# Optimization experiments

Hardware: AMD Instinct MI355X
Metric: run time of the kernel (lower is better)

## Reference

```python
import jax, jax.numpy as jnp
import numpy as np

B, SP, SS = 8, 512, 64          # batch, prefix seq len, suffix seq len
HP, HS = 2048, 1024             # prefix / suffix hidden sizes
NH, NKV, HD = 8, 1, 256         # heads, kv heads, head dim (GQA groups = 8)
IP, IS = 16384, 4096            # MLP intermediate sizes
COND = 1024                     # adaRMSNorm conditioning dim
T = SP + SS
EPS = 1e-6
SCALE = HD ** -0.5
ROPE_BASE = 10000.0


def _rms(x):
    var = jnp.mean(jnp.square(x), axis=-1, keepdims=True)
    return x * jax.lax.rsqrt(var + EPS)


def _rot_half(x):
    x1, x2 = jnp.split(x, 2, axis=-1)
    return jnp.concatenate([-x2, x1], axis=-1)


def setup_inputs() -> dict:
    key = jax.random.key(0)
    ks = iter(jax.random.split(key, 40))
    rn = lambda shape, s=0.02: jax.random.normal(next(ks), shape, dtype=jnp.float32) * s
    return dict(
        x_prefix=rn((B, SP, HP), 1.0),
        x_suffix=rn((B, SS, HS), 1.0),
        cond=rn((B, COND), 1.0),
        attention_mask=jnp.zeros((B, 1, T, T), jnp.float32),
        p_ln1_w=rn((HP,)),
        p_q=rn((NH * HD, HP)), p_k=rn((NKV * HD, HP)), p_v=rn((NKV * HD, HP)), p_o=rn((HP, NH * HD)),
        p_ln2_w=rn((HP,)),
        p_gate=rn((IP, HP)), p_up=rn((IP, HP)), p_down=rn((HP, IP)),
        s_ada1_w=rn((3 * HS, COND)), s_ada1_b=rn((3 * HS,)),
        s_q=rn((NH * HD, HS)), s_k=rn((NKV * HD, HS)), s_v=rn((NKV * HD, HS)), s_o=rn((HS, NH * HD)),
        s_ada2_w=rn((3 * HS, COND)), s_ada2_b=rn((3 * HS,)),
        s_gate=rn((IS, HS)), s_up=rn((IS, HS)), s_down=rn((HS, IS)),
        position_ids=jnp.broadcast_to(jnp.arange(T, dtype=jnp.int32), (B, T)),
    )


def _ada_norm(x, cond, w, b):
    # AdaRMSNormV2: rms(x)*(1+scale)+shift; gate returned separately
    mod = cond @ w.T + b                      # [B, 3*HS]
    scale, shift, gate = jnp.split(mod, 3, axis=-1)
    normed = _rms(x) * (1.0 + scale[:, None, :]) + shift[:, None, :]
    return normed, gate[:, None, :]


def _qkv(h, wq, wk, wv):
    b, t, _ = h.shape
    q = (h @ wq.T).reshape(b, t, NH, HD).transpose(0, 2, 1, 3)   # [B,NH,t,HD]
    k = (h @ wk.T).reshape(b, t, NKV, HD).transpose(0, 2, 1, 3)  # [B,1,t,HD]
    v = (h @ wv.T).reshape(b, t, NKV, HD).transpose(0, 2, 1, 3)
    return q, k, v


def reference(x_prefix, x_suffix, cond, attention_mask,
              p_ln1_w, p_q, p_k, p_v, p_o, p_ln2_w, p_gate, p_up, p_down,
              s_ada1_w, s_ada1_b, s_q, s_k, s_v, s_o, s_ada2_w, s_ada2_b,
              s_gate, s_up, s_down, position_ids):
    # --- pre-attention norms ---
    hp = _rms(x_prefix) * (1.0 + p_ln1_w)                  # plain RMSNorm, gate=None
    hs, gate1 = _ada_norm(x_suffix, cond, s_ada1_w, s_ada1_b)

    qp, kp, vp = _qkv(hp, p_q, p_k, p_v)
    qs, ks, vs = _qkv(hs, s_q, s_k, s_v)
    q = jnp.concatenate([qp, qs], axis=2)                  # [B,NH,T,HD]
    k = jnp.concatenate([kp, ks], axis=2)                  # [B,1,T,HD]
    v = jnp.concatenate([vp, vs], axis=2)

    # --- RoPE over joint sequence ---
    inv_freq = 1.0 / (ROPE_BASE ** (jnp.arange(0, HD, 2, dtype=jnp.float32) / HD))
    freqs = position_ids.astype(jnp.float32)[:, :, None] * inv_freq  # [B,T,HD/2]
    emb = jnp.concatenate([freqs, freqs], axis=-1)
    cos = jnp.cos(emb)[:, None]                            # [B,1,T,HD]
    sin = jnp.sin(emb)[:, None]
    q = q * cos + _rot_half(q) * sin
    k = k * cos + _rot_half(k) * sin

    # --- joint attention (GQA: single kv head broadcast over NH query heads) ---
    k0, v0 = k[:, 0], v[:, 0]                              # [B,T,HD]
    scores = jnp.einsum('bhqd,bkd->bhqk', q, k0) * SCALE
    scores = scores + attention_mask
    probs = jax.nn.softmax(scores, axis=-1)
    attn = jnp.einsum('bhqk,bkd->bhqd', probs, v0)
    attn = attn.transpose(0, 2, 1, 3).reshape(B, T, NH * HD)

    a_p, a_s = attn[:, :SP], attn[:, SP:]

    # --- prefix stream: o_proj + residual + RMSNorm + GeGLU MLP ---
    res_p = x_prefix + a_p @ p_o.T
    h = _rms(res_p) * (1.0 + p_ln2_w)
    mlp_p = (jax.nn.gelu(h @ p_gate.T, approximate=True) * (h @ p_up.T)) @ p_down.T
    out_prefix = res_p + mlp_p

    # --- suffix stream: gated residual + adaRMSNorm + GeGLU MLP + gated residual ---
    res_s = x_suffix + (a_s @ s_o.T) * gate1
    h2, gate2 = _ada_norm(res_s, cond, s_ada2_w, s_ada2_b)
    mlp_s = (jax.nn.gelu(h2 @ s_gate.T, approximate=True) * (h2 @ s_up.T)) @ s_down.T
    out_suffix = res_s + mlp_s * gate2

    return (out_prefix, out_suffix)
```

## Files before the change

### kernel.cpp

```cpp
#include <hip/hip_runtime.h>
#include <cstdint>
#include <cstddef>

typedef __bf16 bf;
typedef __attribute__((ext_vector_type(8))) __bf16 bf16x8;
typedef __attribute__((ext_vector_type(4))) float f32x4;
typedef long long ll;

#define DEV __device__ __forceinline__

constexpr int Tt = 576;
constexpr int NHh = 8;
constexpr float EPSf = 1e-6f;
constexpr float SCALEf = 0.0625f;
constexpr float LN1E4_OVER_128 = 0.07195578515606394f;

constexpr int EPI_F32 = 0, EPI_SCALE_BF16 = 1, EPI_BF16 = 2, EPI_GELU_BF16 = 3,
              EPI_MUL_BF16 = 4, EPI_RES_F32 = 5, EPI_RESGATE_F32 = 6;

DEV float wsum(float v) {
#pragma unroll
  for (int o = 32; o > 0; o >>= 1) v += __shfl_xor(v, o, 64);
  return v;
}
DEV float wmaxr(float v) {
#pragma unroll
  for (int o = 32; o > 0; o >>= 1) v = fmaxf(v, __shfl_xor(v, o, 64));
  return v;
}
DEV float gelu_tanh(float x) {
  float x3 = x * x * x;
  float t = tanhf(0.7978845608028654f * (x + 0.044715f * x3));
  return 0.5f * x * (1.0f + t);
}

DEV void gld16(const void* g, void* l) {
  __builtin_amdgcn_global_load_lds(
      (__attribute__((address_space(1))) void*)(g),
      (__attribute__((address_space(3))) void*)(l), 16, 0, 0);
}


__global__ void f2b_k(const float* __restrict__ s, bf* __restrict__ d, int n8) {
  int i = blockIdx.x * 256 + threadIdx.x;
  int stride = gridDim.x * 256;
  for (; i < n8; i += stride) {
    f32x4 a = ((const f32x4*)s)[i * 2];
    f32x4 b = ((const f32x4*)s)[i * 2 + 1];
    bf16x8 w;
    w[0] = (bf)a[0]; w[1] = (bf)a[1]; w[2] = (bf)a[2]; w[3] = (bf)a[3];
    w[4] = (bf)b[0]; w[5] = (bf)b[1]; w[6] = (bf)b[2]; w[7] = (bf)b[3];
    ((bf16x8*)d)[i] = w;
  }
}

__global__ void rms_scale_2048(const float* __restrict__ x, const float* __restrict__ w,
                               bf* __restrict__ out) {
  int row = blockIdx.x;
  int tid = threadIdx.x;
  const float* xr = x + (ll)row * 2048;
  f32x4 a = *(const f32x4*)(xr + tid * 4);
  f32x4 b = *(const f32x4*)(xr + 1024 + tid * 4);
  float ss = a[0]*a[0]+a[1]*a[1]+a[2]*a[2]+a[3]*a[3]
           + b[0]*b[0]+b[1]*b[1]+b[2]*b[2]+b[3]*b[3];
  ss = wsum(ss);
  __shared__ float red[4];
  if ((tid & 63) == 0) red[tid >> 6] = ss;
  __syncthreads();
  float tot = red[0] + red[1] + red[2] + red[3];
  float sc = rsqrtf(tot * (1.0f / 2048.0f) + EPSf);
  bf* o = out + (ll)row * 2048;
#pragma unroll
  for (int j = 0; j < 4; j++) {
    int c0 = tid * 4 + j;
    o[c0]        = (bf)(a[j] * sc * (1.0f + w[c0]));
    o[1024 + c0] = (bf)(b[j] * sc * (1.0f + w[1024 + c0]));
  }
}

__global__ void ada_mod_k(const float* __restrict__ cond, const float* __restrict__ w,
                          const float* __restrict__ bias, float* __restrict__ mod) {
  int n = blockIdx.x * 256 + threadIdx.x;
  int b = blockIdx.y;
  const float* c = cond + b * 1024;
  const float* wr = w + (ll)n * 1024;
  float s = 0.f;
  for (int k = 0; k < 1024; k += 4) {
    f32x4 cv = *(const f32x4*)(c + k);
    f32x4 wv = *(const f32x4*)(wr + k);
    s += cv[0]*wv[0] + cv[1]*wv[1] + cv[2]*wv[2] + cv[3]*wv[3];
  }
  mod[b * 3072 + n] = s + bias[n];
}

__global__ void ada_norm_k(const float* __restrict__ x, const float* __restrict__ mod,
                           bf* __restrict__ out) {
  int row = blockIdx.x;
  int b = row >> 6;
  int tid = threadIdx.x;
  const float* xr = x + (ll)row * 1024;
  f32x4 a = *(const f32x4*)(xr + tid * 4);
  float ss = a[0]*a[0] + a[1]*a[1] + a[2]*a[2] + a[3]*a[3];
  ss = wsum(ss);
  __shared__ float red[4];
  if ((tid & 63) == 0) red[tid >> 6] = ss;
  __syncthreads();
  float tot = red[0] + red[1] + red[2] + red[3];
  float sc = rsqrtf(tot * (1.0f / 1024.0f) + EPSf);
  const float* m = mod + b * 3072;
  bf* o = out + (ll)row * 1024;
#pragma unroll
  for (int j = 0; j < 4; j++) {
    int c = tid * 4 + j;
    o[c] = (bf)(a[j] * sc * (1.0f + m[c]) + m[1024 + c]);
  }
}

__global__ void rope_k(const float* __restrict__ qbuf, const float* __restrict__ kvbuf,
                       const int* __restrict__ pos, bf* __restrict__ qb,
                       bf* __restrict__ kb, bf* __restrict__ vT) {
  int bt = blockIdx.x;
  int b = bt / Tt, t = bt - b * Tt;
  int tid = threadIdx.x;
  float p = (float)pos[bt];
  const float* qr = qbuf + (ll)bt * 2048;
#pragma unroll
  for (int j = 0; j < 4; j++) {
    int pi = tid + 256 * j;
    int h = pi >> 7, d = pi & 127;
    float ang = p * expf((float)d * (-LN1E4_OVER_128));
    float sn = sinf(ang), cs = cosf(ang);
    float x1 = qr[h * 256 + d], x2 = qr[h * 256 + d + 128];
    bf* qo = qb + ((ll)(b * NHh + h) * Tt + t) * 256;
    qo[d]       = (bf)(x1 * cs - x2 * sn);
    qo[d + 128] = (bf)(x2 * cs + x1 * sn);
  }
  const float* kvr = kvbuf + (ll)bt * 512;
  if (tid < 128) {
    int d = tid;
    float ang = p * expf((float)d * (-LN1E4_OVER_128));
    float sn = sinf(ang), cs = cosf(ang);
    float x1 = kvr[d], x2 = kvr[d + 128];
    bf* ko = kb + (ll)bt * 256;
    ko[d]       = (bf)(x1 * cs - x2 * sn);
    ko[d + 128] = (bf)(x2 * cs + x1 * sn);
  } else {
    int d = tid - 128;
    const float* vv = kvr + 256;
    vT[((ll)b * 256 + d) * Tt + t]       = (bf)vv[d];
    vT[((ll)b * 256 + d + 128) * Tt + t] = (bf)vv[d + 128];
  }
}

__global__ void softmax_k(const bf* __restrict__ scores, const float* __restrict__ mask,
                          bf* __restrict__ probs) {
  int rowg = blockIdx.x * 4 + (threadIdx.x >> 6);
  int lane = threadIdx.x & 63;
  int z = rowg / Tt;
  int t = rowg - z * Tt;
  int b = z >> 3;
  const bf* s = scores + (ll)rowg * Tt;
  const float* mr = mask + ((ll)b * Tt + t) * Tt;
  float v[9];
#pragma unroll
  for (int j = 0; j < 9; j++) {
    int c = lane + j * 64;
    v[j] = (float)s[c] + mr[c];
  }
  float mx = v[0];
#pragma unroll
  for (int j = 1; j < 9; j++) mx = fmaxf(mx, v[j]);
  mx = wmaxr(mx);
  float sum = 0.f;
#pragma unroll
  for (int j = 0; j < 9; j++) { v[j] = __expf(v[j] - mx); sum += v[j]; }
  sum = wsum(sum);
  float inv = 1.0f / sum;
  bf* pr = probs + (ll)rowg * Tt;
#pragma unroll
  for (int j = 0; j < 9; j++) pr[lane + j * 64] = (bf)(v[j] * inv);
}


struct GemmArgs {
  const bf* A; ll sA; int lda;
  const void* Bp; ll sB; int ldb; int zdivB;
  void* C; ll sC; ll sC2; int zdivC; int ldc;
  int M, N, K;
  const float* res; ll sRes;
  const float* gate; ll sGate;
  const bf* aux; ll sAux;
  float alpha;
};

template <int EPI>
DEV void epilogue(const GemmArgs& g, f32x4 (&acc)[4][4], int z, int m0, int n0,
                  int lane, int wr, int wc) {
  const ll coff = (ll)(z / g.zdivC) * g.sC + (ll)(z % g.zdivC) * g.sC2;
  const int r0 = (lane >> 4) * 4;
  const int cc = lane & 15;
#pragma unroll
  for (int m = 0; m < 4; m++) {
#pragma unroll
    for (int n = 0; n < 4; n++) {
      int col = n0 + wc * 64 + n * 16 + cc;
      if (col >= g.N) continue;
#pragma unroll
      for (int r = 0; r < 4; r++) {
        int row = m0 + wr * 64 + m * 16 + r0 + r;
        if (row >= g.M) continue;
        float v = acc[m][n][r];
        ll idx = (ll)row * g.ldc + col;
        if constexpr (EPI == EPI_F32) {
          ((float*)g.C)[coff + idx] = v;
        } else if constexpr (EPI == EPI_SCALE_BF16) {
          ((bf*)g.C)[coff + idx] = (bf)(v * g.alpha);
        } else if constexpr (EPI == EPI_BF16) {
          ((bf*)g.C)[coff + idx] = (bf)v;
        } else if constexpr (EPI == EPI_GELU_BF16) {
          ((bf*)g.C)[coff + idx] = (bf)gelu_tanh(v);
        } else if constexpr (EPI == EPI_MUL_BF16) {
          float a0 = (float)g.aux[(ll)z * g.sAux + idx];
          ((bf*)g.C)[coff + idx] = (bf)(a0 * v);
        } else if constexpr (EPI == EPI_RES_F32) {
          ((float*)g.C)[coff + idx] = g.res[(ll)z * g.sRes + idx] + v;
        } else if constexpr (EPI == EPI_RESGATE_F32) {
          ((float*)g.C)[coff + idx] =
              g.res[(ll)z * g.sRes + idx] + v * g.gate[(ll)z * g.sGate + col];
        }
      }
    }
  }
}

template <int EPI, int BN>
__global__ __launch_bounds__(512) void gemm_8p(GemmArgs g) {
  constexpr int NF = BN / 64;
  constexpr int WN = BN / 4;
  const int z = blockIdx.z;
  const int m0 = blockIdx.x * 256;
  const int n0 = blockIdx.y * BN;
  const int tid = threadIdx.x;
  const int lane = tid & 63;
  const int wv = tid >> 6;
  const int wr = wv >> 2;
  const int wc = wv & 3;

  const bf* A = g.A + (ll)z * g.sA;
  const bf* B = (const bf*)g.Bp + (ll)(z / g.zdivB) * g.sB;

  __shared__ __align__(16) bf lA[2][256 * 64];
  __shared__ __align__(16) bf lB[2][BN * 64];

  f32x4 acc[8][NF];
  f32x4 zero = {0.f, 0.f, 0.f, 0.f};
#pragma unroll
  for (int m = 0; m < 8; m++)
#pragma unroll
    for (int n = 0; n < NF; n++) acc[m][n] = zero;

  const int lrow = lane >> 3;
  const int lsrc = ((lane & 7) ^ lrow) * 8;

  auto stage128 = [&](const bf* src, int ld, int grow0, bf* lds) {
#pragma unroll
    for (int i = 0; i < 2; i++) {
      int chunk = wv * 2 + i;
      gld16(src + (ll)(grow0 + chunk * 8 + lrow) * ld + lsrc, lds + chunk * 512);
    }
  };

  const int NT = g.K >> 6;
  stage128(B, g.ldb, n0, &lB[0][0]);
  if (BN == 256) stage128(B, g.ldb, n0 + 128, &lB[0][128 * 64]);
  stage128(A, g.lda, m0, &lA[0][0]);
  stage128(A, g.lda, m0 + 128, &lA[0][128 * 64]);
  asm volatile("s_waitcnt vmcnt(0)" ::: "memory");
  __builtin_amdgcn_s_barrier();

  for (int t = 0; t < NT; ++t) {
    const int c = t & 1;
    const int nx = (t + 1 < NT) ? t + 1 : t;
    const ll kkn = (ll)nx * 64;
    bf16x8 bv[NF][2];
#pragma unroll
    for (int p = 0; p < 4; ++p) {
      if (p == 0) {
#pragma unroll
        for (int n = 0; n < NF; ++n)
#pragma unroll
          for (int kb = 0; kb < 2; ++kb) {
            int row = wc * WN + n * 16 + (lane & 15);
            int ko = kb * 32 + (lane >> 4) * 8;
            bv[n][kb] = *(const bf16x8*)&lB[c][row * 64 + (ko ^ ((row & 7) * 8))];
          }
      }
      bf16x8 af[2][2];
#pragma unroll
      for (int ml = 0; ml < 2; ++ml)
#pragma unroll
        for (int kb = 0; kb < 2; ++kb) {
          int row = wr * 128 + (2 * p + ml) * 16 + (lane & 15);
          int ko = kb * 32 + (lane >> 4) * 8;
          af[ml][kb] = *(const bf16x8*)&lA[c][row * 64 + (ko ^ ((row & 7) * 8))];
        }
      if (p == 0) {
        stage128(B + kkn, g.ldb, n0, &lB[1 - c][0]);
        if (BN == 256) stage128(B + kkn, g.ldb, n0 + 128, &lB[1 - c][128 * 64]);
      } else if (p == 1) {
        stage128(A + kkn, g.lda, m0, &lA[1 - c][0]);
        stage128(A + kkn, g.lda, m0 + 128, &lA[1 - c][128 * 64]);
      }
      __builtin_amdgcn_s_barrier();
      asm volatile("s_waitcnt lgkmcnt(0)" ::: "memory");
      __builtin_amdgcn_s_setprio(1);
#pragma unroll
      for (int kb = 0; kb < 2; ++kb)
#pragma unroll
        for (int ml = 0; ml < 2; ++ml)
#pragma unroll
          for (int n = 0; n < NF; ++n)
            acc[2 * p + ml][n] = __builtin_amdgcn_mfma_f32_16x16x32_bf16(
                af[ml][kb], bv[n][kb], acc[2 * p + ml][n], 0, 0, 0);
      __builtin_amdgcn_s_setprio(0);
      if (p == 3) asm volatile("s_waitcnt vmcnt(0)" ::: "memory");
      __builtin_amdgcn_s_barrier();
    }
  }

  const ll coff = (ll)(z / g.zdivC) * g.sC + (ll)(z % g.zdivC) * g.sC2;
  const int r0 = (lane >> 4) * 4;
  const int cc = lane & 15;
#pragma unroll
  for (int m = 0; m < 8; m++) {
#pragma unroll
    for (int n = 0; n < NF; n++) {
      int col = n0 + wc * WN + n * 16 + cc;
#pragma unroll
      for (int r = 0; r < 4; r++) {
        int row = m0 + wr * 128 + m * 16 + r0 + r;
        float v = acc[m][n][r];
        ll idx = (ll)row * g.ldc + col;
        if constexpr (EPI == EPI_F32) {
          ((float*)g.C)[coff + idx] = v;
        } else if constexpr (EPI == EPI_GELU_BF16) {
          ((bf*)g.C)[coff + idx] = (bf)gelu_tanh(v);
        } else if constexpr (EPI == EPI_MUL_BF16) {
          float a0 = (float)g.aux[(ll)z * g.sAux + idx];
          ((bf*)g.C)[coff + idx] = (bf)(a0 * v);
        } else if constexpr (EPI == EPI_RES_F32) {
          ((float*)g.C)[coff + idx] = g.res[(ll)z * g.sRes + idx] + v;
        }
      }
    }
  }
}

struct FusedArgs {
  const bf* A; int lda;
  const bf* B1; const bf* B2; int ldb;
  bf* C; int ldc;
  int K;
};

__global__ __launch_bounds__(512) void gemm_8pf(FusedArgs g) {
  const int m0 = blockIdx.x * 256;
  const int n0 = blockIdx.y * 128;
  const int tid = threadIdx.x;
  const int lane = tid & 63;
  const int wv = tid >> 6;
  const int wr = wv >> 2;
  const int wc = wv & 3;

  __shared__ __align__(16) bf lA[2][256 * 64];
  __shared__ __align__(16) bf lB1[2][128 * 64];
  __shared__ __align__(16) bf lB2[2][128 * 64];

  f32x4 acc1[8][2], acc2[8][2];
  f32x4 zero = {0.f, 0.f, 0.f, 0.f};
#pragma unroll
  for (int m = 0; m < 8; m++)
#pragma unroll
    for (int n = 0; n < 2; n++) { acc1[m][n] = zero; acc2[m][n] = zero; }

  const int lrow = lane >> 3;
  const int lsrc = ((lane & 7) ^ lrow) * 8;

  auto stage128 = [&](const bf* src, int ld, int grow0, bf* lds) {
#pragma unroll
    for (int i = 0; i < 2; i++) {
      int chunk = wv * 2 + i;
      gld16(src + (ll)(grow0 + chunk * 8 + lrow) * ld + lsrc, lds + chunk * 512);
    }
  };

  const int NT = g.K >> 6;
  stage128(g.B1, g.ldb, n0, &lB1[0][0]);
  stage128(g.B2, g.ldb, n0, &lB2[0][0]);
  stage128(g.A, g.lda, m0, &lA[0][0]);
  stage128(g.A, g.lda, m0 + 128, &lA[0][128 * 64]);
  asm volatile("s_waitcnt vmcnt(0)" ::: "memory");
  __builtin_amdgcn_s_barrier();

  for (int t = 0; t < NT; ++t) {
    const int c = t & 1;
    const int nx = (t + 1 < NT) ? t + 1 : t;
    const ll kkn = (ll)nx * 64;
    bf16x8 b1v[2][2], b2v[2][2];
#pragma unroll
    for (int p = 0; p < 4; ++p) {
      if (p == 0) {
#pragma unroll
        for (int n = 0; n < 2; ++n)
#pragma unroll
          for (int kb = 0; kb < 2; ++kb) {
            int row = wc * 32 + n * 16 + (lane & 15);
            int ko = kb * 32 + (lane >> 4) * 8;
            int sw = row * 64 + (ko ^ ((row & 7) * 8));
            b1v[n][kb] = *(const bf16x8*)&lB1[c][sw];
            b2v[n][kb] = *(const bf16x8*)&lB2[c][sw];
          }
      }
      bf16x8 af[2][2];
#pragma unroll
      for (int ml = 0; ml < 2; ++ml)
#pragma unroll
        for (int kb = 0; kb < 2; ++kb) {
          int row = wr * 128 + (2 * p + ml) * 16 + (lane & 15);
          int ko = kb * 32 + (lane >> 4) * 8;
          af[ml][kb] = *(const bf16x8*)&lA[c][row * 64 + (ko ^ ((row & 7) * 8))];
        }
      if (p == 0) {
        stage128(g.B1 + kkn, g.ldb, n0, &lB1[1 - c][0]);
        stage128(g.B2 + kkn, g.ldb, n0, &lB2[1 - c][0]);
      } else if (p == 1) {
        stage128(g.A + kkn, g.lda, m0, &lA[1 - c][0]);
        stage128(g.A + kkn, g.lda, m0 + 128, &lA[1 - c][128 * 64]);
      }
      __builtin_amdgcn_s_barrier();
      asm volatile("s_waitcnt lgkmcnt(0)" ::: "memory");
      __builtin_amdgcn_s_setprio(1);
#pragma unroll
      for (int kb = 0; kb < 2; ++kb)
#pragma unroll
        for (int ml = 0; ml < 2; ++ml)
#pragma unroll
          for (int n = 0; n < 2; ++n) {
            acc1[2 * p + ml][n] = __builtin_amdgcn_mfma_f32_16x16x32_bf16(
                af[ml][kb], b1v[n][kb], acc1[2 * p + ml][n], 0, 0, 0);
            acc2[2 * p + ml][n] = __builtin_amdgcn_mfma_f32_16x16x32_bf16(
                af[ml][kb], b2v[n][kb], acc2[2 * p + ml][n], 0, 0, 0);
          }
      __builtin_amdgcn_s_setprio(0);
      if (p == 3) asm volatile("s_waitcnt vmcnt(0)" ::: "memory");
      __builtin_amdgcn_s_barrier();
    }
  }

  const int r0 = (lane >> 4) * 4;
  const int cc = lane & 15;
#pragma unroll
  for (int m = 0; m < 8; m++) {
#pragma unroll
    for (int n = 0; n < 2; n++) {
      int col = n0 + wc * 32 + n * 16 + cc;
#pragma unroll
      for (int r = 0; r < 4; r++) {
        int row = m0 + wr * 128 + m * 16 + r0 + r;
        g.C[(ll)row * g.ldc + col] =
            (bf)(gelu_tanh(acc1[m][n][r]) * acc2[m][n][r]);
      }
    }
  }
}

template <int EPI>
__global__ __launch_bounds__(256) void gemm_p(GemmArgs g) {
  const int z = blockIdx.z;
  const int m0 = blockIdx.x * 128;
  const int n0 = blockIdx.y * 128;
  const int tid = threadIdx.x;
  const int lane = tid & 63;
  const int wid = tid >> 6;
  const int wr = wid >> 1, wc = wid & 1;

  const bf* A = g.A + (ll)z * g.sA;
  const bf* B = (const bf*)g.Bp + (ll)(z / g.zdivB) * g.sB;

  __shared__ __align__(16) bf lA[2][128 * 64];
  __shared__ __align__(16) bf lB[2][128 * 64];

  f32x4 acc[4][4];
  f32x4 zero = {0.f, 0.f, 0.f, 0.f};
#pragma unroll
  for (int m = 0; m < 4; m++)
#pragma unroll
    for (int n = 0; n < 4; n++) acc[m][n] = zero;

  const int lrow = lane >> 3;
  const int lsrc = ((lane & 7) ^ lrow) * 8;

  auto stage = [&](int kt, int bsel) {
    const ll kk = (ll)kt * 64;
#pragma unroll
    for (int i = 0; i < 4; i++) {
      int rr = wid * 32 + i * 8;
      int ra = m0 + rr + lrow; if (ra > g.M - 1) ra = g.M - 1;
      gld16(A + (ll)ra * g.lda + kk + lsrc, &lA[bsel][rr * 64]);
      int rb = n0 + rr + lrow; if (rb > g.N - 1) rb = g.N - 1;
      gld16(B + (ll)rb * g.ldb + kk + lsrc, &lB[bsel][rr * 64]);
    }
  };

  const int nt = g.K >> 6;
  stage(0, 0);
  stage(nt > 1 ? 1 : 0, 1);

  for (int t = 0; t < nt; ++t) {
    const int cur = t & 1;
    asm volatile("s_waitcnt vmcnt(8)" ::: "memory");
    __builtin_amdgcn_s_barrier();
    asm volatile("" ::: "memory");
#pragma unroll
    for (int kb = 0; kb < 2; kb++) {
      const int ko = kb * 32 + (lane >> 4) * 8;
      bf16x8 af[4], bv[4];
#pragma unroll
      for (int m = 0; m < 4; m++) {
        int row = wr * 64 + m * 16 + (lane & 15);
        af[m] = *(const bf16x8*)&lA[cur][row * 64 + (ko ^ ((row & 7) * 8))];
      }
#pragma unroll
      for (int n = 0; n < 4; n++) {
        int row = wc * 64 + n * 16 + (lane & 15);
        bv[n] = *(const bf16x8*)&lB[cur][row * 64 + (ko ^ ((row & 7) * 8))];
      }
      __builtin_amdgcn_s_setprio(1);
#pragma unroll
      for (int m = 0; m < 4; m++)
#pragma unroll
        for (int n = 0; n < 4; n++)
          acc[m][n] = __builtin_amdgcn_mfma_f32_16x16x32_bf16(af[m], bv[n], acc[m][n], 0, 0, 0);
      __builtin_amdgcn_s_setprio(0);
    }
    asm volatile("" ::: "memory");
    __builtin_amdgcn_s_barrier();
    asm volatile("" ::: "memory");
    int nxt = t + 2; if (nxt > nt - 1) nxt = nt - 1;
    stage(nxt, cur);
  }
  epilogue<EPI>(g, acc, z, m0, n0, lane, wr, wc);
}

template <int EPI>
__global__ __launch_bounds__(256) void gemm_rs(GemmArgs g) {
  const int z = blockIdx.z;
  const int m0 = blockIdx.x * 128;
  const int n0 = blockIdx.y * 128;
  const int tid = threadIdx.x;
  const int lane = tid & 63;
  const int wid = tid >> 6;
  const int wr = wid >> 1, wc = wid & 1;

  const bf* A = g.A + (ll)z * g.sA;
  const float* Bf = (const float*)g.Bp + (ll)(z / g.zdivB) * g.sB;

  __shared__ __align__(16) bf lA[128 * 64];
  __shared__ __align__(16) bf lB[128 * 64];

  f32x4 acc[4][4];
  f32x4 zero = {0.f, 0.f, 0.f, 0.f};
#pragma unroll
  for (int m = 0; m < 4; m++)
#pragma unroll
    for (int n = 0; n < 4; n++) acc[m][n] = zero;

  const int srow = tid >> 3;
  const int scol = (tid & 7) * 8;

  for (int kk = 0; kk < g.K; kk += 64) {
#pragma unroll
    for (int i = 0; i < 4; i++) {
      int r = m0 + i * 32 + srow;
      if (r > g.M - 1) r = g.M - 1;
      f32x4 v = *(const f32x4*)(A + (ll)r * g.lda + kk + scol);
      *(f32x4*)&lA[(i * 32 + srow) * 64 + scol] = v;
    }
#pragma unroll
    for (int i = 0; i < 4; i++) {
      int r = n0 + i * 32 + srow;
      if (r > g.N - 1) r = g.N - 1;
      const float* src = Bf + (ll)r * g.ldb + kk + scol;
      f32x4 v0 = *(const f32x4*)(src);
      f32x4 v1 = *(const f32x4*)(src + 4);
      bf16x8 w;
      w[0] = (bf)v0[0]; w[1] = (bf)v0[1]; w[2] = (bf)v0[2]; w[3] = (bf)v0[3];
      w[4] = (bf)v1[0]; w[5] = (bf)v1[1]; w[6] = (bf)v1[2]; w[7] = (bf)v1[3];
      *(bf16x8*)&lB[(i * 32 + srow) * 64 + scol] = w;
    }
    __syncthreads();
#pragma unroll
    for (int kb = 0; kb < 2; kb++) {
      const int ko = kb * 32 + (lane >> 4) * 8;
      bf16x8 af[4], bfv[4];
#pragma unroll
      for (int m = 0; m < 4; m++)
        af[m] = *(const bf16x8*)&lA[(wr * 64 + m * 16 + (lane & 15)) * 64 + ko];
#pragma unroll
      for (int n = 0; n < 4; n++)
        bfv[n] = *(const bf16x8*)&lB[(wc * 64 + n * 16 + (lane & 15)) * 64 + ko];
#pragma unroll
      for (int m = 0; m < 4; m++)
#pragma unroll
        for (int n = 0; n < 4; n++)
          acc[m][n] = __builtin_amdgcn_mfma_f32_16x16x32_bf16(af[m], bfv[n], acc[m][n], 0, 0, 0);
    }
    __syncthreads();
  }
  epilogue<EPI>(g, acc, z, m0, n0, lane, wr, wc);
}


static GemmArgs mkG(const bf* A, ll sA, int lda, const void* Bp, ll sB, int ldb, int zdivB,
                    void* C, ll sC, ll sC2, int zdivC, int ldc, int M, int N, int K) {
  GemmArgs g{};
  g.A = A; g.sA = sA; g.lda = lda;
  g.Bp = Bp; g.sB = sB; g.ldb = ldb; g.zdivB = zdivB;
  g.C = C; g.sC = sC; g.sC2 = sC2; g.zdivC = zdivC; g.ldc = ldc;
  g.M = M; g.N = N; g.K = K;
  g.res = nullptr; g.sRes = 0; g.gate = nullptr; g.sGate = 0; g.aux = nullptr; g.sAux = 0;
  g.alpha = 1.0f;
  return g;
}

extern "C" void kernel_launch(void* const* d_in, const int* in_sizes, int n_in,
                              void* d_out, int out_size, void* d_ws, size_t ws_size,
                              hipStream_t stream) {
  (void)in_sizes; (void)n_in; (void)out_size;
  const float* x_prefix = (const float*)d_in[0];
  const float* x_suffix = (const float*)d_in[1];
  const float* cond     = (const float*)d_in[2];
  const float* mask     = (const float*)d_in[3];
  const float* p_ln1_w  = (const float*)d_in[4];
  const float* p_q      = (const float*)d_in[5];
  const float* p_k      = (const float*)d_in[6];
  const float* p_v      = (const float*)d_in[7];
  const float* p_o      = (const float*)d_in[8];
  const float* p_ln2_w  = (const float*)d_in[9];
  const float* p_gate   = (const float*)d_in[10];
  const float* p_up     = (const float*)d_in[11];
  const float* p_down   = (const float*)d_in[12];
  const float* s_ada1_w = (const float*)d_in[13];
  const float* s_ada1_b = (const float*)d_in[14];
  const float* s_q      = (const float*)d_in[15];
  const float* s_k      = (const float*)d_in[16];
  const float* s_v      = (const float*)d_in[17];
  const float* s_o      = (const float*)d_in[18];
  const float* s_ada2_w = (const float*)d_in[19];
  const float* s_ada2_b = (const float*)d_in[20];
  const float* s_gate   = (const float*)d_in[21];
  const float* s_up     = (const float*)d_in[22];
  const float* s_down   = (const float*)d_in[23];
  const int*   pos      = (const int*)d_in[24];

  char* base = (char*)d_ws;
  size_t off = 0;
  auto alloc = [&](size_t bytes) {
    char* p = base + off;
    off = (off + bytes + 255) & ~(size_t)255;
    return p;
  };
  float* qbuf  = (float*)alloc(8ll * Tt * 2048 * 4);
  float* kvbuf = (float*)alloc(8ll * Tt * 512 * 4);
  bf* hp     = (bf*)alloc(4096ll * 2048 * 2);
  bf* hs     = (bf*)alloc(512ll * 1024 * 2);
  float* mod1 = (float*)alloc(8 * 3072 * 4);
  float* mod2 = (float*)alloc(8 * 3072 * 4);
  bf* qb     = (bf*)alloc(64ll * Tt * 256 * 2);
  bf* kb     = (bf*)alloc(8ll * Tt * 256 * 2);
  bf* vT     = (bf*)alloc(8ll * 256 * Tt * 2);
  bf* scores = (bf*)alloc(64ll * Tt * Tt * 2);
  float* res_p = (float*)alloc(8ll * 512 * 2048 * 4);
  float* res_s = (float*)alloc(8ll * 64 * 1024 * 4);
  bf* gbuf   = (bf*)alloc(4096ll * 16384 * 2);

  bf* attn   = (bf*)qbuf;
  bf* hbuf   = hp;
  bf* h2     = hs;
  bf* probs  = scores;
  bf* gbuf_s = gbuf;

  struct WEnt { const float* src; bf* dst; ll n; };
  WEnt went[14] = {
    {p_q,    nullptr, 2048ll * 2048}, {p_k,    nullptr, 256ll * 2048},
    {p_v,    nullptr, 256ll * 2048},  {p_o,    nullptr, 2048ll * 2048},
    {p_gate, nullptr, 16384ll * 2048},{p_up,   nullptr, 16384ll * 2048},
    {p_down, nullptr, 2048ll * 16384},{s_q,    nullptr, 2048ll * 1024},
    {s_k,    nullptr, 256ll * 1024},  {s_v,    nullptr, 256ll * 1024},
    {s_o,    nullptr, 1024ll * 2048}, {s_gate, nullptr, 4096ll * 1024},
    {s_up,   nullptr, 4096ll * 1024}, {s_down, nullptr, 1024ll * 4096},
  };
  for (int i = 0; i < 14; i++) went[i].dst = (bf*)alloc((size_t)went[i].n * 2);
  const bool conv = (off <= ws_size);

  float* outp = (float*)d_out;
  float* outs = outp + 8ll * 512 * 2048;

  dim3 blk(256);

  if (conv) {
    for (int i = 0; i < 14; i++) {
      int n8 = (int)(went[i].n / 8);
      int grid = (n8 + 255) / 256; if (grid > 4096) grid = 4096;
      f2b_k<<<grid, 256, 0, stream>>>(went[i].src, went[i].dst, n8);
    }
  }
  const bf* w_pq = went[0].dst, *w_pk = went[1].dst, *w_pv = went[2].dst,
          *w_po = went[3].dst, *w_pg = went[4].dst, *w_pu = went[5].dst,
          *w_pd = went[6].dst, *w_sq = went[7].dst, *w_sk = went[8].dst,
          *w_sv = went[9].dst, *w_so = went[10].dst, *w_sg = went[11].dst,
          *w_su = went[12].dst, *w_sd = went[13].dst;

  auto launchW = [&](int epi, GemmArgs g, const float* wf32, const bf* wbf,
                     dim3 grid) {
    if (conv) {
      g.Bp = wbf;
      switch (epi) {
        case EPI_F32:        gemm_p<EPI_F32><<<grid, blk, 0, stream>>>(g); break;
        case EPI_GELU_BF16:  gemm_p<EPI_GELU_BF16><<<grid, blk, 0, stream>>>(g); break;
        case EPI_MUL_BF16:   gemm_p<EPI_MUL_BF16><<<grid, blk, 0, stream>>>(g); break;
        case EPI_RES_F32:    gemm_p<EPI_RES_F32><<<grid, blk, 0, stream>>>(g); break;
        case EPI_RESGATE_F32:gemm_p<EPI_RESGATE_F32><<<grid, blk, 0, stream>>>(g); break;
      }
    } else {
      g.Bp = wf32;
      switch (epi) {
        case EPI_F32:        gemm_rs<EPI_F32><<<grid, blk, 0, stream>>>(g); break;
        case EPI_GELU_BF16:  gemm_rs<EPI_GELU_BF16><<<grid, blk, 0, stream>>>(g); break;
        case EPI_MUL_BF16:   gemm_rs<EPI_MUL_BF16><<<grid, blk, 0, stream>>>(g); break;
        case EPI_RES_F32:    gemm_rs<EPI_RES_F32><<<grid, blk, 0, stream>>>(g); break;
        case EPI_RESGATE_F32:gemm_rs<EPI_RESGATE_F32><<<grid, blk, 0, stream>>>(g); break;
      }
    }
  };

  rms_scale_2048<<<4096, 256, 0, stream>>>(x_prefix, p_ln1_w, hp);
  ada_mod_k<<<dim3(12, 8), 256, 0, stream>>>(cond, s_ada1_w, s_ada1_b, mod1);
  ada_norm_k<<<512, 256, 0, stream>>>(x_suffix, mod1, hs);

  {
    GemmArgs g = mkG(hp, 512ll * 2048, 2048, w_pq, 0, 2048, 1,
                     qbuf, (ll)Tt * 2048, 0, 1, 2048, 512, 2048, 2048);
    if (conv) gemm_8p<EPI_F32, 128><<<dim3(2, 16, 8), 512, 0, stream>>>(g);
    else      launchW(EPI_F32, g, p_q, w_pq, dim3(4, 16, 8));
  }
  launchW(EPI_F32, mkG(hp, 512ll * 2048, 2048, nullptr, 0, 2048, 1,
                       kvbuf, (ll)Tt * 512, 0, 1, 512, 512, 256, 2048),
          p_k, w_pk, dim3(4, 2, 8));
  launchW(EPI_F32, mkG(hp, 512ll * 2048, 2048, nullptr, 0, 2048, 1,
                       kvbuf + 256, (ll)Tt * 512, 0, 1, 512, 512, 256, 2048),
          p_v, w_pv, dim3(4, 2, 8));
  launchW(EPI_F32, mkG(hs, 64ll * 1024, 1024, nullptr, 0, 1024, 1,
                       qbuf + 512ll * 2048, (ll)Tt * 2048, 0, 1, 2048, 64, 2048, 1024),
          s_q, w_sq, dim3(1, 16, 8));
  launchW(EPI_F32, mkG(hs, 64ll * 1024, 1024, nullptr, 0, 1024, 1,
                       kvbuf + 512ll * 512, (ll)Tt * 512, 0, 1, 512, 64, 256, 1024),
          s_k, w_sk, dim3(1, 2, 8));
  launchW(EPI_F32, mkG(hs, 64ll * 1024, 1024, nullptr, 0, 1024, 1,
                       kvbuf + 512ll * 512 + 256, (ll)Tt * 512, 0, 1, 512, 64, 256, 1024),
          s_v, w_sv, dim3(1, 2, 8));
  rope_k<<<8 * Tt, 256, 0, stream>>>(qbuf, kvbuf, pos, qb, kb, vT);

  {
    GemmArgs g = mkG(qb, (ll)Tt * 256, 256, kb, (ll)Tt * 256, 256, 8,
                     scores, (ll)Tt * Tt, 0, 1, Tt, Tt, Tt, 256);
    g.alpha = SCALEf;
    gemm_p<EPI_SCALE_BF16><<<dim3(5, 5, 64), blk, 0, stream>>>(g);
  }
  softmax_k<<<64 * Tt / 4, 256, 0, stream>>>(scores, mask, probs);
  {
    GemmArgs g = mkG(probs, (ll)Tt * Tt, Tt, vT, 256ll * Tt, Tt, 8,
                     attn, (ll)Tt * 2048, 256, 8, 2048, Tt, 256, Tt);
    gemm_p<EPI_BF16><<<dim3(5, 2, 64), blk, 0, stream>>>(g);
  }
  {
    GemmArgs g = mkG(attn, (ll)Tt * 2048, 2048, w_po, 0, 2048, 1,
                     res_p, 512ll * 2048, 0, 1, 2048, 512, 2048, 2048);
    g.res = x_prefix; g.sRes = 512ll * 2048;
    if (conv) gemm_8p<EPI_RES_F32, 128><<<dim3(2, 16, 8), 512, 0, stream>>>(g);
    else      launchW(EPI_RES_F32, g, p_o, w_po, dim3(4, 16, 8));
  }
  {
    GemmArgs g = mkG(attn + 512ll * 2048, (ll)Tt * 2048, 2048, nullptr, 0, 2048, 1,
                     res_s, 64ll * 1024, 0, 1, 1024, 64, 1024, 2048);
    g.res = x_suffix; g.sRes = 64ll * 1024;
    g.gate = mod1 + 2048; g.sGate = 3072;
    launchW(EPI_RESGATE_F32, g, s_o, w_so, dim3(1, 8, 8));
  }
  rms_scale_2048<<<4096, 256, 0, stream>>>(res_p, p_ln2_w, hbuf);
  ada_mod_k<<<dim3(12, 8), 256, 0, stream>>>(cond, s_ada2_w, s_ada2_b, mod2);
  ada_norm_k<<<512, 256, 0, stream>>>(res_s, mod2, h2);

  if (conv) {
    FusedArgs fg{hbuf, 2048, w_pg, w_pu, 2048, gbuf, 16384, 2048};
    gemm_8pf<<<dim3(16, 128, 1), 512, 0, stream>>>(fg);
  } else {
    launchW(EPI_GELU_BF16, mkG(hbuf, 0, 2048, nullptr, 0, 2048, 1,
                               gbuf, 0, 0, 1, 16384, 4096, 16384, 2048),
            p_gate, w_pg, dim3(32, 128, 1));
    GemmArgs g = mkG(hbuf, 0, 2048, nullptr, 0, 2048, 1,
                     gbuf, 0, 0, 1, 16384, 4096, 16384, 2048);
    g.aux = gbuf; g.sAux = 0;
    launchW(EPI_MUL_BF16, g, p_up, w_pu, dim3(32, 128, 1));
  }
  {
    GemmArgs g = mkG(gbuf, 0, 16384, w_pd, 0, 16384, 1,
                     outp, 0, 0, 1, 2048, 4096, 2048, 16384);
    g.res = res_p; g.sRes = 0;
    if (conv) gemm_8p<EPI_RES_F32, 128><<<dim3(16, 16, 1), 512, 0, stream>>>(g);
    else      launchW(EPI_RES_F32, g, p_down, w_pd, dim3(32, 16, 1));
  }
  if (conv) {
    FusedArgs fg{h2, 1024, w_sg, w_su, 1024, gbuf_s, 4096, 1024};
    gemm_8pf<<<dim3(2, 32, 1), 512, 0, stream>>>(fg);
  } else {
    launchW(EPI_GELU_BF16, mkG(h2, 0, 1024, nullptr, 0, 1024, 1,
                               gbuf_s, 0, 0, 1, 4096, 512, 4096, 1024),
            s_gate, w_sg, dim3(4, 32, 1));
    GemmArgs g = mkG(h2, 0, 1024, nullptr, 0, 1024, 1,
                     gbuf_s, 0, 0, 1, 4096, 512, 4096, 1024);
    g.aux = gbuf_s; g.sAux = 0;
    launchW(EPI_MUL_BF16, g, s_up, w_su, dim3(4, 32, 1));
  }
  {
    GemmArgs g = mkG(gbuf_s, 64ll * 4096, 4096, nullptr, 0, 4096, 1,
                     outs, 64ll * 1024, 0, 1, 1024, 64, 1024, 4096);
    g.res = res_s; g.sRes = 64ll * 1024;
    g.gate = mod2 + 2048; g.sGate = 3072;
    launchW(EPI_RESGATE_F32, g, s_down, w_sd, dim3(1, 8, 8));
  }
}
```

Baseline: 1.944 ms.

## Triple-buffer B tiles and swizzle block order in 256-row GEMM kernels

The 256x128 GEMM kernels now keep three LDS buffers for the B operand, prefetching two k-steps ahead, while A stays double-buffered. The vmcnt waits are relaxed so the newest B load can remain in flight across the barrier. The block index is also remapped with a stride-8 swizzle to change how concurrent blocks share A and B tiles in L2/MALL. The cost is more LDS per block (up to 160KB in the fused gate/up kernel) and the removal of the BN=256 and MUL epilogue variants.

```diff
diff --git a/kernel.cpp b/kernel.cpp
--- a/kernel.cpp
+++ b/kernel.cpp
@@ -233,13 +233,16 @@
   }
 }
 
-template <int EPI, int BN>
-__global__ __launch_bounds__(512) void gemm_8p(GemmArgs g) {
-  constexpr int NF = BN / 64;
-  constexpr int WN = BN / 4;
+template <int EPI>
+__global__ __launch_bounds__(512) void gemm_8p3(GemmArgs g) {
   const int z = blockIdx.z;
-  const int m0 = blockIdx.x * 256;
-  const int n0 = blockIdx.y * BN;
+  const int nxy = gridDim.x * gridDim.y;
+  const int lin = blockIdx.x + gridDim.x * blockIdx.y;
+  const int q8 = nxy >> 3;
+  const int swz = (lin & 7) * q8 + (lin >> 3);
+  const int m0 = (swz % gridDim.x) * 256;
+  const int n0 = (swz / gridDim.x) * 128;
+
   const int tid = threadIdx.x;
   const int lane = tid & 63;
   const int wv = tid >> 6;
@@ -250,14 +253,14 @@
   const bf* B = (const bf*)g.Bp + (ll)(z / g.zdivB) * g.sB;
 
   __shared__ __align__(16) bf lA[2][256 * 64];
-  __shared__ __align__(16) bf lB[2][BN * 64];
-
-  f32x4 acc[8][NF];
+  __shared__ __align__(16) bf lB[3][128 * 64];
+
+  f32x4 acc[8][2];
   f32x4 zero = {0.f, 0.f, 0.f, 0.f};
 #pragma unroll
   for (int m = 0; m < 8; m++)
 #pragma unroll
-    for (int n = 0; n < NF; n++) acc[m][n] = zero;
+    for (int n = 0; n < 2; n++) acc[m][n] = zero;
 
   const int lrow = lane >> 3;
   const int lsrc = ((lane & 7) ^ lrow) * 8;
@@ -269,31 +272,43 @@
       gld16(src + (ll)(grow0 + chunk * 8 + lrow) * ld + lsrc, lds + chunk * 512);
     }
   };
+  auto stageA = [&](int kt, int b) {
+    const ll kk = (ll)kt * 64;
+    stage128(A + kk, g.lda, m0, &lA[b][0]);
+    stage128(A + kk, g.lda, m0 + 128, &lA[b][128 * 64]);
+  };
+  auto stageB = [&](int kt, int b) {
+    stage128(B + (ll)kt * 64, g.ldb, n0, &lB[b][0]);
+  };
 
   const int NT = g.K >> 6;
-  stage128(B, g.ldb, n0, &lB[0][0]);
-  if (BN == 256) stage128(B, g.ldb, n0 + 128, &lB[0][128 * 64]);
-  stage128(A, g.lda, m0, &lA[0][0]);
-  stage128(A, g.lda, m0 + 128, &lA[0][128 * 64]);
-  asm volatile("s_waitcnt vmcnt(0)" ::: "memory");
+  stageA(0, 0);
+  stageB(0, 0);
+  stageB(NT > 1 ? 1 : 0, 1);
+  asm volatile("s_waitcnt vmcnt(2)" ::: "memory");
   __builtin_amdgcn_s_barrier();
 
   for (int t = 0; t < NT; ++t) {
     const int c = t & 1;
-    const int nx = (t + 1 < NT) ? t + 1 : t;
-    const ll kkn = (ll)nx * 64;
-    bf16x8 bv[NF][2];
+    const int bc = t % 3;
+    const int bn3 = (t + 2) % 3;
+    const int nxa = (t + 1 < NT) ? t + 1 : NT - 1;
+    const int nxb = (t + 2 < NT) ? t + 2 : NT - 1;
+    bf16x8 bv[2][2];
 #pragma unroll
     for (int p = 0; p < 4; ++p) {
       if (p == 0) {
-#pragma unroll
-        for (int n = 0; n < NF; ++n)
+        stageA(nxa, 1 - c);
+#pragma unroll
+        for (int n = 0; n < 2; ++n)
 #pragma unroll
           for (int kb = 0; kb < 2; ++kb) {
-            int row = wc * WN + n * 16 + (lane & 15);
+            int row = wc * 32 + n * 16 + (lane & 15);
             int ko = kb * 32 + (lane >> 4) * 8;
-            bv[n][kb] = *(const bf16x8*)&lB[c][row * 64 + (ko ^ ((row & 7) * 8))];
+            bv[n][kb] = *(const bf16x8*)&lB[bc][row * 64 + (ko ^ ((row & 7) * 8))];
           }
+      } else if (p == 1) {
+        stageB(nxb, bn3);
       }
       bf16x8 af[2][2];
 #pragma unroll
@@ -304,13 +319,6 @@
           int ko = kb * 32 + (lane >> 4) * 8;
           af[ml][kb] = *(const bf16x8*)&lA[c][row * 64 + (ko ^ ((row & 7) * 8))];
         }
-      if (p == 0) {
-        stage128(B + kkn, g.ldb, n0, &lB[1 - c][0]);
-        if (BN == 256) stage128(B + kkn, g.ldb, n0 + 128, &lB[1 - c][128 * 64]);
-      } else if (p == 1) {
-        stage128(A + kkn, g.lda, m0, &lA[1 - c][0]);
-        stage128(A + kkn, g.lda, m0 + 128, &lA[1 - c][128 * 64]);
-      }
       __builtin_amdgcn_s_barrier();
       asm volatile("s_waitcnt lgkmcnt(0)" ::: "memory");
       __builtin_amdgcn_s_setprio(1);
@@ -319,11 +327,11 @@
 #pragma unroll
         for (int ml = 0; ml < 2; ++ml)
 #pragma unroll
-          for (int n = 0; n < NF; ++n)
+          for (int n = 0; n < 2; ++n)
             acc[2 * p + ml][n] = __builtin_amdgcn_mfma_f32_16x16x32_bf16(
                 af[ml][kb], bv[n][kb], acc[2 * p + ml][n], 0, 0, 0);
       __builtin_amdgcn_s_setprio(0);
-      if (p == 3) asm volatile("s_waitcnt vmcnt(0)" ::: "memory");
+      if (p == 3) asm volatile("s_waitcnt vmcnt(2)" ::: "memory");
       __builtin_amdgcn_s_barrier();
     }
   }
@@ -334,8 +342,8 @@
 #pragma unroll
   for (int m = 0; m < 8; m++) {
 #pragma unroll
-    for (int n = 0; n < NF; n++) {
-      int col = n0 + wc * WN + n * 16 + cc;
+    for (int n = 0; n < 2; n++) {
+      int col = n0 + wc * 32 + n * 16 + cc;
 #pragma unroll
       for (int r = 0; r < 4; r++) {
         int row = m0 + wr * 128 + m * 16 + r0 + r;
@@ -345,9 +353,6 @@
           ((float*)g.C)[coff + idx] = v;
         } else if constexpr (EPI == EPI_GELU_BF16) {
           ((bf*)g.C)[coff + idx] = (bf)gelu_tanh(v);
-        } else if constexpr (EPI == EPI_MUL_BF16) {
-          float a0 = (float)g.aux[(ll)z * g.sAux + idx];
-          ((bf*)g.C)[coff + idx] = (bf)(a0 * v);
         } else if constexpr (EPI == EPI_RES_F32) {
           ((float*)g.C)[coff + idx] = g.res[(ll)z * g.sRes + idx] + v;
         }
@@ -363,9 +368,14 @@
   int K;
 };
 
-__global__ __launch_bounds__(512) void gemm_8pf(FusedArgs g) {
-  const int m0 = blockIdx.x * 256;
-  const int n0 = blockIdx.y * 128;
+__global__ __launch_bounds__(512) void gemm_8pf3(FusedArgs g) {
+  const int nxy = gridDim.x * gridDim.y;
+  const int lin = blockIdx.x + gridDim.x * blockIdx.y;
+  const int q8 = nxy >> 3;
+  const int swz = (lin & 7) * q8 + (lin >> 3);
+  const int m0 = (swz % gridDim.x) * 256;
+  const int n0 = (swz / gridDim.x) * 128;
+
   const int tid = threadIdx.x;
   const int lane = tid & 63;
   const int wv = tid >> 6;
@@ -373,8 +383,8 @@
   const int wc = wv & 3;
 
   __shared__ __align__(16) bf lA[2][256 * 64];
-  __shared__ __align__(16) bf lB1[2][128 * 64];
-  __shared__ __align__(16) bf lB2[2][128 * 64];
+  __shared__ __align__(16) bf lB1[3][128 * 64];
+  __shared__ __align__(16) bf lB2[3][128 * 64];
 
   f32x4 acc1[8][2], acc2[8][2];
   f32x4 zero = {0.f, 0.f, 0.f, 0.f};
@@ -393,23 +403,35 @@
       gld16(src + (ll)(grow0 + chunk * 8 + lrow) * ld + lsrc, lds + chunk * 512);
     }
   };
+  auto stageA = [&](int kt, int b) {
+    const ll kk = (ll)kt * 64;
+    stage128(g.A + kk, g.lda, m0, &lA[b][0]);
+    stage128(g.A + kk, g.lda, m0 + 128, &lA[b][128 * 64]);
+  };
+  auto stageB = [&](int kt, int b) {
+    const ll kk = (ll)kt * 64;
+    stage128(g.B1 + kk, g.ldb, n0, &lB1[b][0]);
+    stage128(g.B2 + kk, g.ldb, n0, &lB2[b][0]);
+  };
 
   const int NT = g.K >> 6;
-  stage128(g.B1, g.ldb, n0, &lB1[0][0]);
-  stage128(g.B2, g.ldb, n0, &lB2[0][0]);
-  stage128(g.A, g.lda, m0, &lA[0][0]);
-  stage128(g.A, g.lda, m0 + 128, &lA[0][128 * 64]);
-  asm volatile("s_waitcnt vmcnt(0)" ::: "memory");
+  stageA(0, 0);
+  stageB(0, 0);
+  stageB(NT > 1 ? 1 : 0, 1);
+  asm volatile("s_waitcnt vmcnt(4)" ::: "memory");
   __builtin_amdgcn_s_barrier();
 
   for (int t = 0; t < NT; ++t) {
     const int c = t & 1;
-    const int nx = (t + 1 < NT) ? t + 1 : t;
-    const ll kkn = (ll)nx * 64;
+    const int bc = t % 3;
+    const int bn3 = (t + 2) % 3;
+    const int nxa = (t + 1 < NT) ? t + 1 : NT - 1;
+    const int nxb = (t + 2 < NT) ? t + 2 : NT - 1;
     bf16x8 b1v[2][2], b2v[2][2];
 #pragma unroll
     for (int p = 0; p < 4; ++p) {
       if (p == 0) {
+        stageA(nxa, 1 - c);
 #pragma unroll
         for (int n = 0; n < 2; ++n)
 #pragma unroll
@@ -417,9 +439,11 @@
             int row = wc * 32 + n * 16 + (lane & 15);
             int ko = kb * 32 + (lane >> 4) * 8;
             int sw = row * 64 + (ko ^ ((row & 7) * 8));
-            b1v[n][kb] = *(const bf16x8*)&lB1[c][sw];
-            b2v[n][kb] = *(const bf16x8*)&lB2[c][sw];
+            b1v[n][kb] = *(const bf16x8*)&lB1[bc][sw];
+            b2v[n][kb] = *(const bf16x8*)&lB2[bc][sw];
           }
+      } else if (p == 1) {
+        stageB(nxb, bn3);
       }
       bf16x8 af[2][2];
 #pragma unroll
@@ -430,13 +454,6 @@
           int ko = kb * 32 + (lane >> 4) * 8;
           af[ml][kb] = *(const bf16x8*)&lA[c][row * 64 + (ko ^ ((row & 7) * 8))];
         }
-      if (p == 0) {
-        stage128(g.B1 + kkn, g.ldb, n0, &lB1[1 - c][0]);
-        stage128(g.B2 + kkn, g.ldb, n0, &lB2[1 - c][0]);
-      } else if (p == 1) {
-        stage128(g.A + kkn, g.lda, m0, &lA[1 - c][0]);
-        stage128(g.A + kkn, g.lda, m0 + 128, &lA[1 - c][128 * 64]);
-      }
       __builtin_amdgcn_s_barrier();
       asm volatile("s_waitcnt lgkmcnt(0)" ::: "memory");
       __builtin_amdgcn_s_setprio(1);
@@ -452,7 +469,7 @@
                 af[ml][kb], b2v[n][kb], acc2[2 * p + ml][n], 0, 0, 0);
           }
       __builtin_amdgcn_s_setprio(0);
-      if (p == 3) asm volatile("s_waitcnt vmcnt(0)" ::: "memory");
+      if (p == 3) asm volatile("s_waitcnt vmcnt(4)" ::: "memory");
       __builtin_amdgcn_s_barrier();
     }
   }
@@ -751,7 +768,7 @@
   {
     GemmArgs g = mkG(hp, 512ll * 2048, 2048, w_pq, 0, 2048, 1,
                      qbuf, (ll)Tt * 2048, 0, 1, 2048, 512, 2048, 2048);
-    if (conv) gemm_8p<EPI_F32, 128><<<dim3(2, 16, 8), 512, 0, stream>>>(g);
+    if (conv) gemm_8p3<EPI_F32><<<dim3(2, 16, 8), 512, 0, stream>>>(g);
     else      launchW(EPI_F32, g, p_q, w_pq, dim3(4, 16, 8));
   }
   launchW(EPI_F32, mkG(hp, 512ll * 2048, 2048, nullptr, 0, 2048, 1,
@@ -787,7 +804,7 @@
     GemmArgs g = mkG(attn, (ll)Tt * 2048, 2048, w_po, 0, 2048, 1,
                      res_p, 512ll * 2048, 0, 1, 2048, 512, 2048, 2048);
     g.res = x_prefix; g.sRes = 512ll * 2048;
-    if (conv) gemm_8p<EPI_RES_F32, 128><<<dim3(2, 16, 8), 512, 0, stream>>>(g);
+    if (conv) gemm_8p3<EPI_RES_F32><<<dim3(2, 16, 8), 512, 0, stream>>>(g);
     else      launchW(EPI_RES_F32, g, p_o, w_po, dim3(4, 16, 8));
   }
   {
@@ -803,7 +820,7 @@
 
   if (conv) {
     FusedArgs fg{hbuf, 2048, w_pg, w_pu, 2048, gbuf, 16384, 2048};
-    gemm_8pf<<<dim3(16, 128, 1), 512, 0, stream>>>(fg);
+    gemm_8pf3<<<dim3(16, 128, 1), 512, 0, stream>>>(fg);
   } else {
     launchW(EPI_GELU_BF16, mkG(hbuf, 0, 2048, nullptr, 0, 2048, 1,
                                gbuf, 0, 0, 1, 16384, 4096, 16384, 2048),
@@ -817,12 +834,12 @@
     GemmArgs g = mkG(gbuf, 0, 16384, w_pd, 0, 16384, 1,
                      outp, 0, 0, 1, 2048, 4096, 2048, 16384);
     g.res = res_p; g.sRes = 0;
-    if (conv) gemm_8p<EPI_RES_F32, 128><<<dim3(16, 16, 1), 512, 0, stream>>>(g);
+    if (conv) gemm_8p3<EPI_RES_F32><<<dim3(16, 16, 1), 512, 0, stream>>>(g);
     else      launchW(EPI_RES_F32, g, p_down, w_pd, dim3(32, 16, 1));
   }
   if (conv) {
     FusedArgs fg{h2, 1024, w_sg, w_su, 1024, gbuf_s, 4096, 1024};
-    gemm_8pf<<<dim3(2, 32, 1), 512, 0, stream>>>(fg);
+    gemm_8pf3<<<dim3(2, 32, 1), 512, 0, stream>>>(fg);
   } else {
     launchW(EPI_GELU_BF16, mkG(h2, 0, 1024, nullptr, 0, 1024, 1,
                                gbuf_s, 0, 0, 1, 4096, 512, 4096, 1024),
```

Result: slower. 2.421 ms (+24.5%).

## Fuse Q/K/V projections into single GEMMs and merge GEMM staging phases

Applied to the files above, without the earlier changes.

Concatenates the Q, K and V weights so each stream's QKV projection runs as one GEMM writing a combined 2560-wide buffer, replacing three separate launches per stream. RoPE now reads q and kv from that fused buffer. The GEMM main loops also issue the A-tile staging loads together with the B-tile loads in phase 0 instead of spreading them over two phases. This cuts launch count and gives better tile occupancy for the small K/V projections. It relies on the converted weights being laid out contiguously, and the changed staging may shift memory/compute overlap.

```diff
diff --git a/kernel.cpp b/kernel.cpp
--- a/kernel.cpp
+++ b/kernel.cpp
@@ -116,14 +116,14 @@
   }
 }
 
-__global__ void rope_k(const float* __restrict__ qbuf, const float* __restrict__ kvbuf,
+__global__ void rope_k(const float* __restrict__ qkv,
                        const int* __restrict__ pos, bf* __restrict__ qb,
                        bf* __restrict__ kb, bf* __restrict__ vT) {
   int bt = blockIdx.x;
   int b = bt / Tt, t = bt - b * Tt;
   int tid = threadIdx.x;
   float p = (float)pos[bt];
-  const float* qr = qbuf + (ll)bt * 2048;
+  const float* qr = qkv + (ll)bt * 2560;
 #pragma unroll
   for (int j = 0; j < 4; j++) {
     int pi = tid + 256 * j;
@@ -135,7 +135,7 @@
     qo[d]       = (bf)(x1 * cs - x2 * sn);
     qo[d + 128] = (bf)(x2 * cs + x1 * sn);
   }
-  const float* kvr = kvbuf + (ll)bt * 512;
+  const float* kvr = qr + 2048;
   if (tid < 128) {
     int d = tid;
     float ang = p * expf((float)d * (-LN1E4_OVER_128));
@@ -307,7 +307,6 @@
       if (p == 0) {
         stage128(B + kkn, g.ldb, n0, &lB[1 - c][0]);
         if (BN == 256) stage128(B + kkn, g.ldb, n0 + 128, &lB[1 - c][128 * 64]);
-      } else if (p == 1) {
         stage128(A + kkn, g.lda, m0, &lA[1 - c][0]);
         stage128(A + kkn, g.lda, m0 + 128, &lA[1 - c][128 * 64]);
       }
@@ -433,7 +432,6 @@
       if (p == 0) {
         stage128(g.B1 + kkn, g.ldb, n0, &lB1[1 - c][0]);
         stage128(g.B2 + kkn, g.ldb, n0, &lB2[1 - c][0]);
-      } else if (p == 1) {
         stage128(g.A + kkn, g.lda, m0, &lA[1 - c][0]);
         stage128(g.A + kkn, g.lda, m0 + 128, &lA[1 - c][128 * 64]);
       }
@@ -670,8 +668,7 @@
     off = (off + bytes + 255) & ~(size_t)255;
     return p;
   };
-  float* qbuf  = (float*)alloc(8ll * Tt * 2048 * 4);
-  float* kvbuf = (float*)alloc(8ll * Tt * 512 * 4);
+  float* qkv   = (float*)alloc(8ll * Tt * 2560 * 4);
   bf* hp     = (bf*)alloc(4096ll * 2048 * 2);
   bf* hs     = (bf*)alloc(512ll * 1024 * 2);
   float* mod1 = (float*)alloc(8 * 3072 * 4);
@@ -684,7 +681,7 @@
   float* res_s = (float*)alloc(8ll * 64 * 1024 * 4);
   bf* gbuf   = (bf*)alloc(4096ll * 16384 * 2);
 
-  bf* attn   = (bf*)qbuf;
+  bf* attn   = (bf*)qkv;
   bf* hbuf   = hp;
   bf* h2     = hs;
   bf* probs  = scores;
@@ -715,10 +712,11 @@
       f2b_k<<<grid, 256, 0, stream>>>(went[i].src, went[i].dst, n8);
     }
   }
-  const bf* w_pq = went[0].dst, *w_pk = went[1].dst, *w_pv = went[2].dst,
-          *w_po = went[3].dst, *w_pg = went[4].dst, *w_pu = went[5].dst,
-          *w_pd = went[6].dst, *w_sq = went[7].dst, *w_sk = went[8].dst,
-          *w_sv = went[9].dst, *w_so = went[10].dst, *w_sg = went[11].dst,
+  const bf* w_pqkv = went[0].dst;
+  const bf* w_po = went[3].dst, *w_pg = went[4].dst, *w_pu = went[5].dst,
+          *w_pd = went[6].dst;
+  const bf* w_sqkv = went[7].dst;
+  const bf* w_so = went[10].dst, *w_sg = went[11].dst,
           *w_su = went[12].dst, *w_sd = went[13].dst;
 
   auto launchW = [&](int epi, GemmArgs g, const float* wf32, const bf* wbf,
@@ -748,28 +746,37 @@
   ada_mod_k<<<dim3(12, 8), 256, 0, stream>>>(cond, s_ada1_w, s_ada1_b, mod1);
   ada_norm_k<<<512, 256, 0, stream>>>(x_suffix, mod1, hs);
 
-  {
-    GemmArgs g = mkG(hp, 512ll * 2048, 2048, w_pq, 0, 2048, 1,
-                     qbuf, (ll)Tt * 2048, 0, 1, 2048, 512, 2048, 2048);
-    if (conv) gemm_8p<EPI_F32, 128><<<dim3(2, 16, 8), 512, 0, stream>>>(g);
-    else      launchW(EPI_F32, g, p_q, w_pq, dim3(4, 16, 8));
-  }
-  launchW(EPI_F32, mkG(hp, 512ll * 2048, 2048, nullptr, 0, 2048, 1,
-                       kvbuf, (ll)Tt * 512, 0, 1, 512, 512, 256, 2048),
-          p_k, w_pk, dim3(4, 2, 8));
-  launchW(EPI_F32, mkG(hp, 512ll * 2048, 2048, nullptr, 0, 2048, 1,
-                       kvbuf + 256, (ll)Tt * 512, 0, 1, 512, 512, 256, 2048),
-          p_v, w_pv, dim3(4, 2, 8));
-  launchW(EPI_F32, mkG(hs, 64ll * 1024, 1024, nullptr, 0, 1024, 1,
-                       qbuf + 512ll * 2048, (ll)Tt * 2048, 0, 1, 2048, 64, 2048, 1024),
-          s_q, w_sq, dim3(1, 16, 8));
-  launchW(EPI_F32, mkG(hs, 64ll * 1024, 1024, nullptr, 0, 1024, 1,
-                       kvbuf + 512ll * 512, (ll)Tt * 512, 0, 1, 512, 64, 256, 1024),
-          s_k, w_sk, dim3(1, 2, 8));
-  launchW(EPI_F32, mkG(hs, 64ll * 1024, 1024, nullptr, 0, 1024, 1,
-                       kvbuf + 512ll * 512 + 256, (ll)Tt * 512, 0, 1, 512, 64, 256, 1024),
-          s_v, w_sv, dim3(1, 2, 8));
-  rope_k<<<8 * Tt, 256, 0, stream>>>(qbuf, kvbuf, pos, qb, kb, vT);
+  if (conv) {
+    GemmArgs g = mkG(hp, 512ll * 2048, 2048, w_pqkv, 0, 2048, 1,
+                     qkv, (ll)Tt * 2560, 0, 1, 2560, 512, 2560, 2048);
+    gemm_8p<EPI_F32, 128><<<dim3(2, 20, 8), 512, 0, stream>>>(g);
+  } else {
+    launchW(EPI_F32, mkG(hp, 512ll * 2048, 2048, nullptr, 0, 2048, 1,
+                         qkv, (ll)Tt * 2560, 0, 1, 2560, 512, 2048, 2048),
+            p_q, nullptr, dim3(4, 16, 8));
+    launchW(EPI_F32, mkG(hp, 512ll * 2048, 2048, nullptr, 0, 2048, 1,
+                         qkv + 2048, (ll)Tt * 2560, 0, 1, 2560, 512, 256, 2048),
+            p_k, nullptr, dim3(4, 2, 8));
+    launchW(EPI_F32, mkG(hp, 512ll * 2048, 2048, nullptr, 0, 2048, 1,
+                         qkv + 2304, (ll)Tt * 2560, 0, 1, 2560, 512, 256, 2048),
+            p_v, nullptr, dim3(4, 2, 8));
+  }
+  if (conv) {
+    GemmArgs g = mkG(hs, 64ll * 1024, 1024, w_sqkv, 0, 1024, 1,
+                     qkv + 512ll * 2560, (ll)Tt * 2560, 0, 1, 2560, 64, 2560, 1024);
+    gemm_p<EPI_F32><<<dim3(1, 20, 8), blk, 0, stream>>>(g);
+  } else {
+    launchW(EPI_F32, mkG(hs, 64ll * 1024, 1024, nullptr, 0, 1024, 1,
+                         qkv + 512ll * 2560, (ll)Tt * 2560, 0, 1, 2560, 64, 2048, 1024),
+            s_q, nullptr, dim3(1, 16, 8));
+    launchW(EPI_F32, mkG(hs, 64ll * 1024, 1024, nullptr, 0, 1024, 1,
+                         qkv + 512ll * 2560 + 2048, (ll)Tt * 2560, 0, 1, 2560, 64, 256, 1024),
+            s_k, nullptr, dim3(1, 2, 8));
+    launchW(EPI_F32, mkG(hs, 64ll * 1024, 1024, nullptr, 0, 1024, 1,
+                         qkv + 512ll * 2560 + 2304, (ll)Tt * 2560, 0, 1, 2560, 64, 256, 1024),
+            s_v, nullptr, dim3(1, 2, 8));
+  }
+  rope_k<<<8 * Tt, 256, 0, stream>>>(qkv, pos, qb, kb, vT);
 
   {
     GemmArgs g = mkG(qb, (ll)Tt * 256, 256, kb, (ll)Tt * 256, 256, 8,
```

New measurement: 1.962 ms. No clear change (+0.9%).
